# Performance work log

Hardware: AMD Instinct MI355X
Metric: run time of the kernel (lower is better)

## Reference

```python
import jax, jax.numpy as jnp
import numpy as np


def setup_inputs() -> dict:
    key = jax.random.key(0)
    k1, k2 = jax.random.split(key)
    B, N, d = 8, 4096, 256
    S_pred = jax.random.normal(k1, (B, N, d), dtype=jnp.float32)
    # binary adjacency in {0,1}; nonzero entries define neighbors
    adjacency = jax.random.randint(k2, (N, N), 0, 2, dtype=jnp.int32)
    return {"S_pred": S_pred, "adjacency": adjacency}


def reference(S_pred, adjacency):
    # S_pred: (B, N, d), adjacency: (N, N)
    B, N, d = S_pred.shape
    A = (adjacency != 0).astype(S_pred.dtype)          # (N, N) binary
    deg = A.sum(axis=1)                                 # (N,) neighbor counts
    # neighbor mean: (A @ S) / deg  -> per node i, mean over j in N(i) of S_j
    neigh_sum = jnp.einsum('ij,bjd->bid', A, S_pred)   # (B, N, d)
    neigh_mean = neigh_sum / jnp.maximum(deg, 1.0)[None, :, None]
    # div_i = mean_j (S_j - S_i) = neigh_mean_i - S_i; zero for isolated nodes
    div = neigh_mean - S_pred                           # (B, N, d)
    mask = (deg > 0).astype(S_pred.dtype)[None, :, None]
    divergence = jnp.sum((div * mask) ** 2) / (B * N * d)
    return divergence
```

## Files before the change

### kernel.cpp

```cpp
#include <hip/hip_runtime.h>
#include <stdint.h>

#define N_NODES 4096
#define DMODEL  256
#define BATCH   8
#define NCOL    (BATCH * DMODEL)
#define KDIM    N_NODES
#define INV_BND (1.0f / 8388608.0f)

typedef __attribute__((ext_vector_type(8))) int   int32x8;
typedef __attribute__((ext_vector_type(4))) float f32x4;

__device__ __forceinline__ void async_load16(const void* g, void* l) {
  __builtin_amdgcn_global_load_lds(
      (const __attribute__((address_space(1))) void*)g,
      (__attribute__((address_space(3))) void*)l, 16, 0, 0);
}

__device__ __forceinline__ f32x4 mfma_mx(int32x8 a, int32x8 b, f32x4 c) {
  return __builtin_amdgcn_mfma_scale_f32_16x16x128_f8f6f4(
      a, b, c, 0, 0, 0, 0x7F7F7F7Fu, 0, 0x7F7F7F7Fu);
}

__global__ __launch_bounds__(256) void fat_prep(const int* __restrict__ adj,
                                                const float* __restrict__ S,
                                                unsigned char* __restrict__ A8,
                                                unsigned char* __restrict__ B8,
                                                float* __restrict__ w,
                                                float* __restrict__ out) {
  __shared__ float tile[128][36];
  __shared__ int wred[4];
  const int bx = blockIdx.x;
  const int t  = threadIdx.x;

  if (bx < N_NODES) {
    if (bx == 0 && t == 0) *out = 0.0f;
    const int4* arow = (const int4*)(adj + (size_t)bx * N_NODES);
    int cnt = 0;
    unsigned int b[4];
#pragma unroll
    for (int q = 0; q < 4; ++q) {
      int4 a = arow[t * 4 + q];
      unsigned int p = 0;
      p |= a.x ? 0x38u       : 0u; cnt += (a.x != 0);
      p |= a.y ? 0x3800u     : 0u; cnt += (a.y != 0);
      p |= a.z ? 0x380000u   : 0u; cnt += (a.z != 0);
      p |= a.w ? 0x38000000u : 0u; cnt += (a.w != 0);
      b[q] = p;
    }
    uint4 o; o.x = b[0]; o.y = b[1]; o.z = b[2]; o.w = b[3];
    ((uint4*)(A8 + (size_t)bx * N_NODES))[t] = o;
#pragma unroll
    for (int off = 32; off > 0; off >>= 1) cnt += __shfl_down(cnt, off);
    if ((t & 63) == 0) wred[t >> 6] = cnt;
    __syncthreads();
    if (t == 0) {
      int total = wred[0] + wred[1] + wred[2] + wred[3];
      w[bx] = (total > 0) ? (1.0f / (float)total) : 0.0f;
    }
  } else {
    const int bt = bx - N_NODES;
    const int j0 = (bt & 31) * 128;
    const int d0 = ((bt >> 5) & 7) * 32;
    const int bb = bt >> 8;
    const float* Sb = S + (size_t)bb * (N_NODES * DMODEL);

#pragma unroll
    for (int p = 0; p < 4; ++p) {
      const int idx = p * 256 + t;
      const int j = idx >> 3;
      const int c = idx & 7;
      float4 v = *(const float4*)&Sb[(size_t)(j0 + j) * DMODEL + d0 + c * 4];
      *(float4*)&tile[j][c * 4] = v;
    }
    __syncthreads();

    const int dr = t >> 3;
    const int jt = (t & 7) * 16;
    uint4 o;
    {
      int v0 = __builtin_amdgcn_cvt_pk_fp8_f32(tile[jt + 0][dr], tile[jt + 1][dr], 0, false);
      v0     = __builtin_amdgcn_cvt_pk_fp8_f32(tile[jt + 2][dr], tile[jt + 3][dr], v0, true);
      int v1 = __builtin_amdgcn_cvt_pk_fp8_f32(tile[jt + 4][dr], tile[jt + 5][dr], 0, false);
      v1     = __builtin_amdgcn_cvt_pk_fp8_f32(tile[jt + 6][dr], tile[jt + 7][dr], v1, true);
      int v2 = __builtin_amdgcn_cvt_pk_fp8_f32(tile[jt + 8][dr], tile[jt + 9][dr], 0, false);
      v2     = __builtin_amdgcn_cvt_pk_fp8_f32(tile[jt +10][dr], tile[jt +11][dr], v2, true);
      int v3 = __builtin_amdgcn_cvt_pk_fp8_f32(tile[jt +12][dr], tile[jt +13][dr], 0, false);
      v3     = __builtin_amdgcn_cvt_pk_fp8_f32(tile[jt +14][dr], tile[jt +15][dr], v3, true);
      o.x = (unsigned int)v0; o.y = (unsigned int)v1;
      o.z = (unsigned int)v2; o.w = (unsigned int)v3;
    }
    *(uint4*)&B8[(size_t)(bb * DMODEL + d0 + dr) * KDIM + j0 + jt] = o;
  }
}

__global__ __launch_bounds__(256, 4) void gemm_div(const unsigned char* __restrict__ A8,
                                                   const unsigned char* __restrict__ B8,
                                                   const float* __restrict__ w,
                                                   const float* __restrict__ S,
                                                   float* __restrict__ out) {
  __shared__ unsigned char As[16384];
  __shared__ unsigned char Bs[16384];
  __shared__ float wsum[4];

  const int tid  = threadIdx.x;
  const int lane = tid & 63;
  const int wave = tid >> 6;
  const int wm   = wave >> 1;
  const int wn   = wave & 1;
  const int l16  = lane & 15;
  const int quad = lane >> 4;

  const int rowBase = blockIdx.x * 128;
  const int colBase = blockIdx.y * 128;

  const int srow = lane >> 3;
  const int kc   = ((lane & 7) ^ srow) * 16;

  f32x4 acc[4][4];
  const f32x4 zero = {0.f, 0.f, 0.f, 0.f};
#pragma unroll
  for (int i = 0; i < 4; ++i)
#pragma unroll
    for (int j = 0; j < 4; ++j) acc[i][j] = zero;

  const unsigned char* Ag = A8 + (size_t)rowBase * KDIM;
  const unsigned char* Bg = B8 + (size_t)colBase * KDIM;

  for (int k0 = 0; k0 < KDIM; k0 += 128) {
#pragma unroll
    for (int c = 0; c < 4; ++c) {
      const int ch = wave * 4 + c;
      const int r  = ch * 8 + srow;
      async_load16(Ag + (size_t)r * KDIM + k0 + kc, As + ch * 1024);
      async_load16(Bg + (size_t)r * KDIM + k0 + kc, Bs + ch * 1024);
    }
    __syncthreads();

    int32x8 bfrag[4];
#pragma unroll
    for (int nt = 0; nt < 4; ++nt) {
      const int r = wn * 64 + nt * 16 + l16;
      const unsigned char* rp = Bs + r * 128;
      const int x = r & 7;
      int4 lo = *(const int4*)(rp + (((2 * quad)    ) ^ x) * 16);
      int4 hi = *(const int4*)(rp + (((2 * quad) | 1) ^ x) * 16);
      bfrag[nt][0] = lo.x; bfrag[nt][1] = lo.y; bfrag[nt][2] = lo.z; bfrag[nt][3] = lo.w;
      bfrag[nt][4] = hi.x; bfrag[nt][5] = hi.y; bfrag[nt][6] = hi.z; bfrag[nt][7] = hi.w;
    }
#pragma unroll
    for (int mt = 0; mt < 4; ++mt) {
      const int r = wm * 64 + mt * 16 + l16;
      const unsigned char* rp = As + r * 128;
      const int x = r & 7;
      int4 lo = *(const int4*)(rp + (((2 * quad)    ) ^ x) * 16);
      int4 hi = *(const int4*)(rp + (((2 * quad) | 1) ^ x) * 16);
      int32x8 a;
      a[0] = lo.x; a[1] = lo.y; a[2] = lo.z; a[3] = lo.w;
      a[4] = hi.x; a[5] = hi.y; a[6] = hi.z; a[7] = hi.w;
#pragma unroll
      for (int nt = 0; nt < 4; ++nt)
        acc[mt][nt] = mfma_mx(a, bfrag[nt], acc[mt][nt]);
    }
    __syncthreads();
  }

  float local = 0.0f;
#pragma unroll
  for (int mt = 0; mt < 4; ++mt) {
    const int i0 = rowBase + wm * 64 + mt * 16 + quad * 4;
    float wr[4];
#pragma unroll
    for (int r = 0; r < 4; ++r) wr[r] = w[i0 + r];
#pragma unroll
    for (int nt = 0; nt < 4; ++nt) {
      const int col = colBase + wn * 64 + nt * 16 + l16;
      const int bb = col >> 8;
      const int dd = col & 255;
      const float* Sp = S + (size_t)bb * (N_NODES * DMODEL) + (size_t)i0 * DMODEL + dd;
#pragma unroll
      for (int r = 0; r < 4; ++r) {
        float v = acc[mt][nt][r] * wr[r] - Sp[(size_t)r * DMODEL];
        v = (wr[r] > 0.0f) ? v : 0.0f;
        local += v * v;
      }
    }
  }

#pragma unroll
  for (int off = 32; off > 0; off >>= 1) local += __shfl_down(local, off);
  if (lane == 0) wsum[wave] = local;
  __syncthreads();
  if (tid == 0)
    atomicAdd(out, (wsum[0] + wsum[1] + wsum[2] + wsum[3]) * INV_BND);
}

extern "C" void kernel_launch(void* const* d_in, const int* in_sizes, int n_in,
                              void* d_out, int out_size, void* d_ws, size_t ws_size,
                              hipStream_t stream) {
  const float* S  = (const float*)d_in[0];
  const int* adj  = (const int*)d_in[1];
  float* out = (float*)d_out;

  unsigned char* A8 = (unsigned char*)d_ws;
  unsigned char* B8 = (unsigned char*)d_ws + (size_t)N_NODES * N_NODES;
  float* w = (float*)((char*)d_ws + (size_t)N_NODES * N_NODES + (size_t)NCOL * KDIM);

  fat_prep<<<N_NODES + (N_NODES / 128) * (DMODEL / 32) * BATCH, 256, 0, stream>>>(
      adj, S, A8, B8, w, out);

  gemm_div<<<dim3(N_NODES / 128, NCOL / 128, 1), 256, 0, stream>>>(A8, B8, w, S, out);
}
```

Measured before the change: 163.3 us.

## Load B fragments directly from global and shrink row tile to 64

The GEMM kernel stops staging B in shared memory. Each wave loads its B fragments straight from global memory into registers, while A is still staged through LDS with a 256-wide K step and a 16-way XOR swizzle. The block tile shrinks from 128x128 to 64x128, which doubles the grid and halves the accumulators per wave. The aim is to cut LDS traffic and footprint and raise occupancy, at the cost of uncoalesced direct global B loads that are repeated across waves and blocks.

```diff
diff --git a/kernel.cpp b/kernel.cpp
--- a/kernel.cpp
+++ b/kernel.cpp
@@ -20,6 +20,13 @@
 __device__ __forceinline__ f32x4 mfma_mx(int32x8 a, int32x8 b, f32x4 c) {
   return __builtin_amdgcn_mfma_scale_f32_16x16x128_f8f6f4(
       a, b, c, 0, 0, 0, 0x7F7F7F7Fu, 0, 0x7F7F7F7Fu);
+}
+
+__device__ __forceinline__ int32x8 pack_frag(int4 lo, int4 hi) {
+  int32x8 f;
+  f[0] = lo.x; f[1] = lo.y; f[2] = lo.z; f[3] = lo.w;
+  f[4] = hi.x; f[5] = hi.y; f[6] = hi.z; f[7] = hi.w;
+  return f;
 }
 
 __global__ __launch_bounds__(256) void fat_prep(const int* __restrict__ adj,
@@ -99,8 +106,7 @@
                                                    const float* __restrict__ w,
                                                    const float* __restrict__ S,
                                                    float* __restrict__ out) {
-  __shared__ unsigned char As[16384];
-  __shared__ unsigned char Bs[16384];
+  __shared__ unsigned char As[64 * 256];
   __shared__ float wsum[4];
 
   const int tid  = threadIdx.x;
@@ -111,64 +117,77 @@
   const int l16  = lane & 15;
   const int quad = lane >> 4;
 
-  const int rowBase = blockIdx.x * 128;
+  const int rowBase = blockIdx.x * 64;
   const int colBase = blockIdx.y * 128;
 
-  const int srow = lane >> 3;
-  const int kc   = ((lane & 7) ^ srow) * 16;
-
-  f32x4 acc[4][4];
+  const unsigned char* Ag = A8 + (size_t)rowBase * KDIM;
+
+  const unsigned char* Bcol[4];
+#pragma unroll
+  for (int nt = 0; nt < 4; ++nt)
+    Bcol[nt] = B8 + (size_t)(colBase + wn * 64 + nt * 16 + l16) * KDIM + quad * 32;
+
+  const int srow_in = lane >> 4;
+  const int spos    = lane & 15;
+
+  f32x4 acc[2][4];
   const f32x4 zero = {0.f, 0.f, 0.f, 0.f};
 #pragma unroll
-  for (int i = 0; i < 4; ++i)
+  for (int i = 0; i < 2; ++i)
 #pragma unroll
     for (int j = 0; j < 4; ++j) acc[i][j] = zero;
 
-  const unsigned char* Ag = A8 + (size_t)rowBase * KDIM;
-  const unsigned char* Bg = B8 + (size_t)colBase * KDIM;
-
-  for (int k0 = 0; k0 < KDIM; k0 += 128) {
+  for (int k0 = 0; k0 < KDIM; k0 += 256) {
+    int4 b0lo[4], b0hi[4];
+#pragma unroll
+    for (int nt = 0; nt < 4; ++nt) {
+      b0lo[nt] = *(const int4*)(Bcol[nt] + k0);
+      b0hi[nt] = *(const int4*)(Bcol[nt] + k0 + 16);
+    }
 #pragma unroll
     for (int c = 0; c < 4; ++c) {
-      const int ch = wave * 4 + c;
-      const int r  = ch * 8 + srow;
-      async_load16(Ag + (size_t)r * KDIM + k0 + kc, As + ch * 1024);
-      async_load16(Bg + (size_t)r * KDIM + k0 + kc, Bs + ch * 1024);
-    }
-    __syncthreads();
-
-    int32x8 bfrag[4];
+      const int row = wave * 16 + c * 4 + srow_in;
+      async_load16(Ag + (size_t)row * KDIM + k0 + ((spos ^ (row & 15)) * 16),
+                   As + (wave * 16 + c * 4) * 256);
+    }
+    __syncthreads();
+
+    int4 b1lo[4], b1hi[4];
 #pragma unroll
     for (int nt = 0; nt < 4; ++nt) {
-      const int r = wn * 64 + nt * 16 + l16;
-      const unsigned char* rp = Bs + r * 128;
-      const int x = r & 7;
-      int4 lo = *(const int4*)(rp + (((2 * quad)    ) ^ x) * 16);
-      int4 hi = *(const int4*)(rp + (((2 * quad) | 1) ^ x) * 16);
-      bfrag[nt][0] = lo.x; bfrag[nt][1] = lo.y; bfrag[nt][2] = lo.z; bfrag[nt][3] = lo.w;
-      bfrag[nt][4] = hi.x; bfrag[nt][5] = hi.y; bfrag[nt][6] = hi.z; bfrag[nt][7] = hi.w;
-    }
-#pragma unroll
-    for (int mt = 0; mt < 4; ++mt) {
-      const int r = wm * 64 + mt * 16 + l16;
-      const unsigned char* rp = As + r * 128;
-      const int x = r & 7;
-      int4 lo = *(const int4*)(rp + (((2 * quad)    ) ^ x) * 16);
-      int4 hi = *(const int4*)(rp + (((2 * quad) | 1) ^ x) * 16);
-      int32x8 a;
-      a[0] = lo.x; a[1] = lo.y; a[2] = lo.z; a[3] = lo.w;
-      a[4] = hi.x; a[5] = hi.y; a[6] = hi.z; a[7] = hi.w;
-#pragma unroll
-      for (int nt = 0; nt < 4; ++nt)
-        acc[mt][nt] = mfma_mx(a, bfrag[nt], acc[mt][nt]);
+      b1lo[nt] = *(const int4*)(Bcol[nt] + k0 + 128);
+      b1hi[nt] = *(const int4*)(Bcol[nt] + k0 + 144);
+    }
+
+#pragma unroll
+    for (int s = 0; s < 2; ++s) {
+      int32x8 afrag[2];
+#pragma unroll
+      for (int mt = 0; mt < 2; ++mt) {
+        const int r = wm * 32 + mt * 16 + l16;
+        const unsigned char* rp = As + r * 256;
+        const int x = r & 15;
+        const int c0 = s * 8 + 2 * quad;
+        int4 lo = *(const int4*)(rp + ((c0    ) ^ x) * 16);
+        int4 hi = *(const int4*)(rp + ((c0 | 1) ^ x) * 16);
+        afrag[mt] = pack_frag(lo, hi);
+      }
+#pragma unroll
+      for (int nt = 0; nt < 4; ++nt) {
+        int32x8 bf = s ? pack_frag(b1lo[nt], b1hi[nt])
+                       : pack_frag(b0lo[nt], b0hi[nt]);
+#pragma unroll
+        for (int mt = 0; mt < 2; ++mt)
+          acc[mt][nt] = mfma_mx(afrag[mt], bf, acc[mt][nt]);
+      }
     }
     __syncthreads();
   }
 
   float local = 0.0f;
 #pragma unroll
-  for (int mt = 0; mt < 4; ++mt) {
-    const int i0 = rowBase + wm * 64 + mt * 16 + quad * 4;
+  for (int mt = 0; mt < 2; ++mt) {
+    const int i0 = rowBase + wm * 32 + mt * 16 + quad * 4;
     float wr[4];
 #pragma unroll
     for (int r = 0; r < 4; ++r) wr[r] = w[i0 + r];
@@ -209,5 +228,5 @@
   fat_prep<<<N_NODES + (N_NODES / 128) * (DMODEL / 32) * BATCH, 256, 0, stream>>>(
       adj, S, A8, B8, w, out);
 
-  gemm_div<<<dim3(N_NODES / 128, NCOL / 128, 1), 256, 0, stream>>>(A8, B8, w, S, out);
-}
+  gemm_div<<<dim3(N_NODES / 64, NCOL / 128, 1), 256, 0, stream>>>(A8, B8, w, S, out);
+}
```

Result: slower. 242.3 us (+48.4%).

## Switch GEMM operands to FP4 with MFMA-fragment-ordered prepacked panels

Applied to the files above, without the earlier changes.

Quantizes both the adjacency and S to FP4 (e2m1) instead of FP8 and prepacks them into panels already laid out in MFMA fragment order. The GEMM then loads fragments straight from global memory into registers with double buffering, dropping LDS staging and block barriers, and each wave does its own atomic. The aim is to halve operand bytes, use the faster FP4 MFMA rate, and cut LDS and sync overhead. The cost is much coarser quantization of S (only 8 magnitude levels), which may push the result past tolerance, plus lower occupancy hinted by launch bounds and more atomics.

```diff
diff --git a/kernel.cpp b/kernel.cpp
--- a/kernel.cpp
+++ b/kernel.cpp
@@ -11,55 +11,72 @@
 typedef __attribute__((ext_vector_type(8))) int   int32x8;
 typedef __attribute__((ext_vector_type(4))) float f32x4;
 
-__device__ __forceinline__ void async_load16(const void* g, void* l) {
-  __builtin_amdgcn_global_load_lds(
-      (const __attribute__((address_space(1))) void*)g,
-      (__attribute__((address_space(3))) void*)l, 16, 0, 0);
-}
-
-__device__ __forceinline__ f32x4 mfma_mx(int32x8 a, int32x8 b, f32x4 c) {
+__device__ __forceinline__ f32x4 mfma_fp4(int4 a, int4 b, f32x4 c) {
+  int32x8 av = {a.x, a.y, a.z, a.w, 0, 0, 0, 0};
+  int32x8 bv = {b.x, b.y, b.z, b.w, 0, 0, 0, 0};
   return __builtin_amdgcn_mfma_scale_f32_16x16x128_f8f6f4(
-      a, b, c, 0, 0, 0, 0x7F7F7F7Fu, 0, 0x7F7F7F7Fu);
-}
+      av, bv, c, 4, 4, 0, 0x7F7F7F7Fu, 0, 0x7F7F7F7Fu);
+}
+
+__device__ __forceinline__ unsigned int fp4_enc(float x) {
+  float ax = fabsf(x);
+  unsigned int m = (ax >= 0.25f) + (ax >= 0.75f) + (ax >= 1.25f) + (ax >= 1.75f)
+                 + (ax >= 2.5f)  + (ax >= 3.5f)  + (ax >= 5.0f);
+  return m | (x < 0.0f ? 8u : 0u);
+}
+
 
 __global__ __launch_bounds__(256) void fat_prep(const int* __restrict__ adj,
                                                 const float* __restrict__ S,
-                                                unsigned char* __restrict__ A8,
-                                                unsigned char* __restrict__ B8,
+                                                unsigned char* __restrict__ A4,
+                                                unsigned char* __restrict__ B4,
                                                 float* __restrict__ w,
                                                 float* __restrict__ out) {
-  __shared__ float tile[128][36];
-  __shared__ int wred[4];
   const int bx = blockIdx.x;
   const int t  = threadIdx.x;
 
-  if (bx < N_NODES) {
+  if (bx < N_NODES / 16) {
+    __shared__ int deg[16];
+    if (t < 16) deg[t] = 0;
     if (bx == 0 && t == 0) *out = 0.0f;
-    const int4* arow = (const int4*)(adj + (size_t)bx * N_NODES);
+    __syncthreads();
+
+    const int rt   = bx;
+    const int row  = t & 15;
+    const int quad = (t >> 4) & 3;
+    const int t6   = t >> 6;
+    const size_t rowg = (size_t)rt * 16 + row;
+    const int4* base = (const int4*)adj + rowg * 1024;
+    unsigned char* opan = A4 + (size_t)rt * 32768;
     int cnt = 0;
-    unsigned int b[4];
-#pragma unroll
-    for (int q = 0; q < 4; ++q) {
-      int4 a = arow[t * 4 + q];
-      unsigned int p = 0;
-      p |= a.x ? 0x38u       : 0u; cnt += (a.x != 0);
-      p |= a.y ? 0x3800u     : 0u; cnt += (a.y != 0);
-      p |= a.z ? 0x380000u   : 0u; cnt += (a.z != 0);
-      p |= a.w ? 0x38000000u : 0u; cnt += (a.w != 0);
-      b[q] = p;
-    }
-    uint4 o; o.x = b[0]; o.y = b[1]; o.z = b[2]; o.w = b[3];
-    ((uint4*)(A8 + (size_t)bx * N_NODES))[t] = o;
-#pragma unroll
-    for (int off = 32; off > 0; off >>= 1) cnt += __shfl_down(cnt, off);
-    if ((t & 63) == 0) wred[t >> 6] = cnt;
+#pragma unroll
+    for (int p = 0; p < 8; ++p) {
+      const int kt = 4 * p + t6;
+      const int4* src = base + kt * 32 + quad * 8;
+      unsigned int dw[4];
+#pragma unroll
+      for (int d = 0; d < 4; ++d) {
+        int4 a = src[2 * d];
+        int4 b = src[2 * d + 1];
+        dw[d] = (a.x ? 0x2u : 0u) | (a.y ? 0x20u : 0u) |
+                (a.z ? 0x200u : 0u) | (a.w ? 0x2000u : 0u) |
+                (b.x ? 0x20000u : 0u) | (b.y ? 0x200000u : 0u) |
+                (b.z ? 0x2000000u : 0u) | (b.w ? 0x20000000u : 0u);
+        cnt += (a.x != 0) + (a.y != 0) + (a.z != 0) + (a.w != 0) +
+               (b.x != 0) + (b.y != 0) + (b.z != 0) + (b.w != 0);
+      }
+      uint4 o; o.x = dw[0]; o.y = dw[1]; o.z = dw[2]; o.w = dw[3];
+      *(uint4*)(opan + p * 4096 + t * 16) = o;
+    }
+    atomicAdd(&deg[row], cnt);
     __syncthreads();
-    if (t == 0) {
-      int total = wred[0] + wred[1] + wred[2] + wred[3];
-      w[bx] = (total > 0) ? (1.0f / (float)total) : 0.0f;
+    if (t < 16) {
+      int d = deg[t];
+      w[rt * 16 + t] = (d > 0) ? (1.0f / (float)d) : 0.0f;
     }
   } else {
-    const int bt = bx - N_NODES;
+    __shared__ float tile[128][36];
+    const int bt = bx - N_NODES / 16;
     const int j0 = (bt & 31) * 128;
     const int d0 = ((bt >> 5) & 7) * 32;
     const int bb = bt >> 8;
@@ -75,47 +92,40 @@
     }
     __syncthreads();
 
-    const int dr = t >> 3;
-    const int jt = (t & 7) * 16;
-    uint4 o;
-    {
-      int v0 = __builtin_amdgcn_cvt_pk_fp8_f32(tile[jt + 0][dr], tile[jt + 1][dr], 0, false);
-      v0     = __builtin_amdgcn_cvt_pk_fp8_f32(tile[jt + 2][dr], tile[jt + 3][dr], v0, true);
-      int v1 = __builtin_amdgcn_cvt_pk_fp8_f32(tile[jt + 4][dr], tile[jt + 5][dr], 0, false);
-      v1     = __builtin_amdgcn_cvt_pk_fp8_f32(tile[jt + 6][dr], tile[jt + 7][dr], v1, true);
-      int v2 = __builtin_amdgcn_cvt_pk_fp8_f32(tile[jt + 8][dr], tile[jt + 9][dr], 0, false);
-      v2     = __builtin_amdgcn_cvt_pk_fp8_f32(tile[jt +10][dr], tile[jt +11][dr], v2, true);
-      int v3 = __builtin_amdgcn_cvt_pk_fp8_f32(tile[jt +12][dr], tile[jt +13][dr], 0, false);
-      v3     = __builtin_amdgcn_cvt_pk_fp8_f32(tile[jt +14][dr], tile[jt +15][dr], v3, true);
-      o.x = (unsigned int)v0; o.y = (unsigned int)v1;
-      o.z = (unsigned int)v2; o.w = (unsigned int)v3;
-    }
-    *(uint4*)&B8[(size_t)(bb * DMODEL + d0 + dr) * KDIM + j0 + jt] = o;
-  }
-}
-
-__global__ __launch_bounds__(256, 4) void gemm_div(const unsigned char* __restrict__ A8,
-                                                   const unsigned char* __restrict__ B8,
+    const int ct_i  = t >> 7;
+    const int lane2 = (t & 127) >> 1;
+    const int col16 = lane2 & 15;
+    const int q2    = lane2 >> 4;
+    const int half  = t & 1;
+    const int cl    = ct_i * 16 + col16;
+    const int jb    = q2 * 32 + half * 16;
+    unsigned int dw0 = 0, dw1 = 0;
+#pragma unroll
+    for (int i = 0; i < 8; ++i) dw0 |= fp4_enc(tile[jb + i][cl]) << (4 * i);
+#pragma unroll
+    for (int i = 0; i < 8; ++i) dw1 |= fp4_enc(tile[jb + 8 + i][cl]) << (4 * i);
+    uint2 o; o.x = dw0; o.y = dw1;
+    const size_t ct = (size_t)bb * 16 + ((bt >> 5) & 7) * 2 + ct_i;
+    *(uint2*)(B4 + ct * 32768 + (size_t)(bt & 31) * 1024 + lane2 * 16 + half * 8) = o;
+  }
+}
+
+__global__ __launch_bounds__(256, 2) void gemm_div(const unsigned char* __restrict__ A4,
+                                                   const unsigned char* __restrict__ B4,
                                                    const float* __restrict__ w,
                                                    const float* __restrict__ S,
                                                    float* __restrict__ out) {
-  __shared__ unsigned char As[16384];
-  __shared__ unsigned char Bs[16384];
-  __shared__ float wsum[4];
-
   const int tid  = threadIdx.x;
   const int lane = tid & 63;
   const int wave = tid >> 6;
-  const int wm   = wave >> 1;
-  const int wn   = wave & 1;
   const int l16  = lane & 15;
   const int quad = lane >> 4;
 
-  const int rowBase = blockIdx.x * 128;
-  const int colBase = blockIdx.y * 128;
-
-  const int srow = lane >> 3;
-  const int kc   = ((lane & 7) ^ srow) * 16;
+  const int rowBase = blockIdx.x * 128 + (wave >> 1) * 64;
+  const int colBase = blockIdx.y * 128 + (wave & 1) * 64;
+
+  const unsigned char* Ap = A4 + (size_t)(rowBase >> 4) * 32768 + lane * 16;
+  const unsigned char* Bp = B4 + (size_t)(colBase >> 4) * 32768 + lane * 16;
 
   f32x4 acc[4][4];
   const f32x4 zero = {0.f, 0.f, 0.f, 0.f};
@@ -124,57 +134,41 @@
 #pragma unroll
     for (int j = 0; j < 4; ++j) acc[i][j] = zero;
 
-  const unsigned char* Ag = A8 + (size_t)rowBase * KDIM;
-  const unsigned char* Bg = B8 + (size_t)colBase * KDIM;
-
-  for (int k0 = 0; k0 < KDIM; k0 += 128) {
-#pragma unroll
-    for (int c = 0; c < 4; ++c) {
-      const int ch = wave * 4 + c;
-      const int r  = ch * 8 + srow;
-      async_load16(Ag + (size_t)r * KDIM + k0 + kc, As + ch * 1024);
-      async_load16(Bg + (size_t)r * KDIM + k0 + kc, Bs + ch * 1024);
-    }
-    __syncthreads();
-
-    int32x8 bfrag[4];
+  int4 af[2][4], bfr[2][4];
+#pragma unroll
+  for (int r = 0; r < 4; ++r) {
+    af[0][r]  = *(const int4*)(Ap + (size_t)r * 32768);
+    bfr[0][r] = *(const int4*)(Bp + (size_t)r * 32768);
+  }
+
+#pragma unroll
+  for (int kt = 0; kt < 32; ++kt) {
+    const int cur = kt & 1, nxt = cur ^ 1;
+    if (kt < 31) {
+      const int o = (kt + 1) * 1024;
+#pragma unroll
+      for (int r = 0; r < 4; ++r) {
+        af[nxt][r]  = *(const int4*)(Ap + (size_t)r * 32768 + o);
+        bfr[nxt][r] = *(const int4*)(Bp + (size_t)r * 32768 + o);
+      }
+    }
+#pragma unroll
+    for (int mt = 0; mt < 4; ++mt)
+#pragma unroll
+      for (int nt = 0; nt < 4; ++nt)
+        acc[mt][nt] = mfma_fp4(af[cur][mt], bfr[cur][nt], acc[mt][nt]);
+  }
+
+  float local = 0.0f;
+#pragma unroll
+  for (int mt = 0; mt < 4; ++mt) {
+    const int i0 = rowBase + mt * 16 + quad * 4;
+    float wr[4];
+#pragma unroll
+    for (int r = 0; r < 4; ++r) wr[r] = w[i0 + r];
 #pragma unroll
     for (int nt = 0; nt < 4; ++nt) {
-      const int r = wn * 64 + nt * 16 + l16;
-      const unsigned char* rp = Bs + r * 128;
-      const int x = r & 7;
-      int4 lo = *(const int4*)(rp + (((2 * quad)    ) ^ x) * 16);
-      int4 hi = *(const int4*)(rp + (((2 * quad) | 1) ^ x) * 16);
-      bfrag[nt][0] = lo.x; bfrag[nt][1] = lo.y; bfrag[nt][2] = lo.z; bfrag[nt][3] = lo.w;
-      bfrag[nt][4] = hi.x; bfrag[nt][5] = hi.y; bfrag[nt][6] = hi.z; bfrag[nt][7] = hi.w;
-    }
-#pragma unroll
-    for (int mt = 0; mt < 4; ++mt) {
-      const int r = wm * 64 + mt * 16 + l16;
-      const unsigned char* rp = As + r * 128;
-      const int x = r & 7;
-      int4 lo = *(const int4*)(rp + (((2 * quad)    ) ^ x) * 16);
-      int4 hi = *(const int4*)(rp + (((2 * quad) | 1) ^ x) * 16);
-      int32x8 a;
-      a[0] = lo.x; a[1] = lo.y; a[2] = lo.z; a[3] = lo.w;
-      a[4] = hi.x; a[5] = hi.y; a[6] = hi.z; a[7] = hi.w;
-#pragma unroll
-      for (int nt = 0; nt < 4; ++nt)
-        acc[mt][nt] = mfma_mx(a, bfrag[nt], acc[mt][nt]);
-    }
-    __syncthreads();
-  }
-
-  float local = 0.0f;
-#pragma unroll
-  for (int mt = 0; mt < 4; ++mt) {
-    const int i0 = rowBase + wm * 64 + mt * 16 + quad * 4;
-    float wr[4];
-#pragma unroll
-    for (int r = 0; r < 4; ++r) wr[r] = w[i0 + r];
-#pragma unroll
-    for (int nt = 0; nt < 4; ++nt) {
-      const int col = colBase + wn * 64 + nt * 16 + l16;
+      const int col = colBase + nt * 16 + l16;
       const int bb = col >> 8;
       const int dd = col & 255;
       const float* Sp = S + (size_t)bb * (N_NODES * DMODEL) + (size_t)i0 * DMODEL + dd;
@@ -189,10 +183,7 @@
 
 #pragma unroll
   for (int off = 32; off > 0; off >>= 1) local += __shfl_down(local, off);
-  if (lane == 0) wsum[wave] = local;
-  __syncthreads();
-  if (tid == 0)
-    atomicAdd(out, (wsum[0] + wsum[1] + wsum[2] + wsum[3]) * INV_BND);
+  if (lane == 0) atomicAdd(out, local * INV_BND);
 }
 
 extern "C" void kernel_launch(void* const* d_in, const int* in_sizes, int n_in,
@@ -202,12 +193,12 @@
   const int* adj  = (const int*)d_in[1];
   float* out = (float*)d_out;
 
-  unsigned char* A8 = (unsigned char*)d_ws;
-  unsigned char* B8 = (unsigned char*)d_ws + (size_t)N_NODES * N_NODES;
-  float* w = (float*)((char*)d_ws + (size_t)N_NODES * N_NODES + (size_t)NCOL * KDIM);
-
-  fat_prep<<<N_NODES + (N_NODES / 128) * (DMODEL / 32) * BATCH, 256, 0, stream>>>(
-      adj, S, A8, B8, w, out);
-
-  gemm_div<<<dim3(N_NODES / 128, NCOL / 128, 1), 256, 0, stream>>>(A8, B8, w, S, out);
-}
+  unsigned char* A4 = (unsigned char*)d_ws;
+  unsigned char* B4 = (unsigned char*)d_ws + (size_t)N_NODES * N_NODES / 2;
+  float* w = (float*)((char*)d_ws + (size_t)N_NODES * N_NODES / 2
+                                  + (size_t)NCOL * KDIM / 2);
+
+  fat_prep<<<N_NODES / 16 + 32 * 8 * BATCH, 256, 0, stream>>>(adj, S, A4, B4, w, out);
+
+  gemm_div<<<dim3(N_NODES / 128, NCOL / 128, 1), 256, 0, stream>>>(A4, B4, w, S, out);
+}
```

Measured after the change: 190.5 us. 1.17x slower.
